# Performance work log

Hardware: AMD Instinct MI355X
Metric: run time of the kernel (lower is better)

Reference implementation:

```python
import jax, jax.numpy as jnp
import numpy as np

B, H, W, C = 64, 56, 56, 128
WIN, SHIFT, NH = 7, 3, 4
HD = C // NH
N = WIN * WIN
HID = 4 * C
EPS = 1e-5


def _rel_index():
    coords = np.stack(np.meshgrid(np.arange(WIN), np.arange(WIN), indexing='ij')).reshape(2, -1)
    rel = coords[:, :, None] - coords[:, None, :]
    rel = rel.transpose(1, 2, 0).astype(np.int64)
    rel[..., 0] += WIN - 1
    rel[..., 1] += WIN - 1
    rel[..., 0] *= 2 * WIN - 1
    return rel.sum(-1)  # [N, N]


def _attn_mask():
    img = np.zeros((H, W), dtype=np.float32)
    cnt = 0
    bounds = [(0, H - WIN), (H - WIN, H - SHIFT), (H - SHIFT, H)]
    for h0, h1 in bounds:
        for w0, w1 in bounds:
            img[h0:h1, w0:w1] = cnt
            cnt += 1
    mw = img.reshape(H // WIN, WIN, W // WIN, WIN).transpose(0, 2, 1, 3).reshape(-1, N)
    am = mw[:, None, :] - mw[:, :, None]
    return np.where(am != 0, -100.0, 0.0).astype(np.float32)  # [nW, N, N]


def setup_inputs() -> dict:
    key = jax.random.key(0)
    ks = jax.random.split(key, 16)
    s = lambda k, shp, f: (jax.random.normal(k, shp, jnp.float32) * f)
    return {
        'x': s(ks[0], (B, H * W, C), 1.0),
        'norm1_w': jnp.ones((C,), jnp.float32),
        'norm1_b': jnp.zeros((C,), jnp.float32),
        'qkv_w': s(ks[1], (3 * C, C), 0.02),
        'qkv_b': jnp.zeros((3 * C,), jnp.float32),
        'proj_w': s(ks[2], (C, C), 0.02),
        'proj_b': jnp.zeros((C,), jnp.float32),
        'norm2_w': jnp.ones((C,), jnp.float32),
        'norm2_b': jnp.zeros((C,), jnp.float32),
        'fc1_w': s(ks[3], (HID, C), 0.02),
        'fc1_b': jnp.zeros((HID,), jnp.float32),
        'fc2_w': s(ks[4], (C, HID), 0.02),
        'fc2_b': jnp.zeros((C,), jnp.float32),
        'bias_table': s(ks[5], ((2 * WIN - 1) ** 2, NH), 0.02),
        'attn_mask': jnp.asarray(_attn_mask()),
        'rel_index': jnp.asarray(_rel_index(), jnp.int32),
    }


def _ln(x, w, b):
    mu = x.mean(-1, keepdims=True)
    var = ((x - mu) ** 2).mean(-1, keepdims=True)
    return (x - mu) * jax.lax.rsqrt(var + EPS) * w + b


def reference(x, norm1_w, norm1_b, qkv_w, qkv_b, proj_w, proj_b,
              norm2_w, norm2_b, fc1_w, fc1_b, fc2_w, fc2_b,
              bias_table, attn_mask, rel_index):
    Bx, L, Cx = x.shape
    shortcut = x
    xn = _ln(x, norm1_w, norm1_b).reshape(Bx, H, W, Cx)
    xs = jnp.roll(xn, (-SHIFT, -SHIFT), axis=(1, 2))
    # window partition -> [B*nW, N, C]
    xw = xs.reshape(Bx, H // WIN, WIN, W // WIN, WIN, Cx).transpose(0, 1, 3, 2, 4, 5).reshape(-1, N, Cx)
    B_ = xw.shape[0]
    qkv = (xw @ qkv_w.T + qkv_b).reshape(B_, N, 3, NH, HD).transpose(2, 0, 3, 1, 4)
    q, k, v = qkv[0], qkv[1], qkv[2]
    q = q * (HD ** -0.5)
    attn = jnp.einsum('bhnd,bhmd->bhnm', q, k)  # [B_, NH, N, N]
    bias = bias_table[rel_index.reshape(-1)].reshape(N, N, NH).transpose(2, 0, 1)
    attn = attn + bias[None]
    nW = attn_mask.shape[0]
    attn = attn.reshape(B_ // nW, nW, NH, N, N) + attn_mask[None, :, None]
    attn = jax.nn.softmax(attn.reshape(B_, NH, N, N), axis=-1)
    out = jnp.einsum('bhnm,bhmd->bhnd', attn, v).transpose(0, 2, 1, 3).reshape(B_, N, Cx)
    out = out @ proj_w.T + proj_b
    # window reverse + roll back
    out = out.reshape(Bx, H // WIN, W // WIN, WIN, WIN, Cx).transpose(0, 1, 3, 2, 4, 5).reshape(Bx, H, W, Cx)
    out = jnp.roll(out, (SHIFT, SHIFT), axis=(1, 2)).reshape(Bx, L, Cx)
    x = shortcut + out
    h = _ln(x, norm2_w, norm2_b)
    h = jax.nn.gelu(h @ fc1_w.T + fc1_b, approximate=False) @ fc2_w.T + fc2_b
    return x + h
```

## Files before the change

kernel.cpp:

```cpp
#include <hip/hip_runtime.h>
#include <hip/hip_bf16.h>
#include <stdint.h>

typedef unsigned int uint;
typedef unsigned short ushort;
typedef short s16x8 __attribute__((ext_vector_type(8)));
typedef float f32x4 __attribute__((ext_vector_type(4)));

#define DEV static __device__ __forceinline__

DEV float bflo(uint u){ union{uint i;float f;} v; v.i = u<<16; return v.f; }
DEV float bfhi(uint u){ union{uint i;float f;} v; v.i = u & 0xffff0000u; return v.f; }
DEV float bf2f(ushort u){ union{uint i;float f;} v; v.i = ((uint)u)<<16; return v.f; }
DEV ushort f2bf(float f){ union{float f;uint i;} v; v.f=f; uint r=(v.i + 0x7fffu + ((v.i>>16)&1u))>>16; return (ushort)r; }

DEV f32x4 MFMA_BF(s16x8 a, s16x8 b, f32x4 c){
  return __builtin_amdgcn_mfma_f32_16x16x32_bf16(a, b, c, 0, 0, 0);
}

DEV float ld1(const void* b, int i, bool f32){
  return f32 ? ((const float*)b)[i] : bf2f(((const ushort*)b)[i]);
}
DEV ushort ld_bf(const void* b, int i, bool f32){
  return f32 ? f2bf(((const float*)b)[i]) : ((const ushort*)b)[i];
}
DEV void ld2(const void* b, int i, bool f32, float& a0, float& a1){
  if(f32){ float2 t = *(const float2*)((const float*)b + i); a0=t.x; a1=t.y; }
  else   { uint p = *(const uint*)((const ushort*)b + i); a0=bflo(p); a1=bfhi(p); }
}
DEV void ld8(const void* b, int i, bool f32, float* f){
  if(f32){
    const float* p = (const float*)b + i;
    float4 a0 = *(const float4*)p, a1 = *(const float4*)(p+4);
    f[0]=a0.x; f[1]=a0.y; f[2]=a0.z; f[3]=a0.w;
    f[4]=a1.x; f[5]=a1.y; f[6]=a1.z; f[7]=a1.w;
  } else {
    uint4 p = *(const uint4*)((const ushort*)b + i);
    f[0]=bflo(p.x); f[1]=bfhi(p.x); f[2]=bflo(p.y); f[3]=bfhi(p.y);
    f[4]=bflo(p.z); f[5]=bfhi(p.z); f[6]=bflo(p.w); f[7]=bfhi(p.w);
  }
}
DEV void st1(void* b, int i, bool f32, float v){
  if(f32) ((float*)b)[i] = v; else ((ushort*)b)[i] = f2bf(v);
}
DEV bool probe_f32(const void* normw){ return *(const uint*)normw == 0x3F800000u; }
DEV float clamp1k(float v){ return fminf(fmaxf(v, -1024.f), 1024.f); }

DEV float gelu_fast(float a){
  float t = a*(0.79788456080286536f + 0.035677408136300125f*a*a);
  float e = __expf(2.f*t);
  float th = 1.f - 2.f/(e+1.f);
  return 0.5f*a*(1.f+th);
}


__global__ void swin_prep(const void* __restrict__ n1w,
                          const void* __restrict__ qkvw, const void* __restrict__ projw,
                          const void* __restrict__ btab, const int* __restrict__ ridx,
                          const void* __restrict__ amask,
                          const void* __restrict__ fc1w, const void* __restrict__ fc2w,
                          ushort* __restrict__ qkvw_r, ushort* __restrict__ projw_r,
                          ushort* __restrict__ comb_t, ushort* __restrict__ amask_t,
                          ushort* __restrict__ fc1w_r, ushort* __restrict__ fc2w_r)
{
  const bool f32 = probe_f32(n1w);
  int idx=blockIdx.x*256+threadIdx.x;
  if(idx<49152){
    int j=idx&7, l=(idx>>3)&63, rest=idx>>9, ks=rest&3, nt=rest>>2;
    qkvw_r[idx]=ld_bf(qkvw, (nt*16+(l&15))*128 + ks*32 + (l>>4)*8 + j, f32);
  }
  if(idx<16384){
    int j=idx&7, l=(idx>>3)&63, rest=idx>>9, ks=rest&3, nt=rest>>2;
    projw_r[idx]=ld_bf(projw, (nt*16+(l&15))*128 + ks*32 + (l>>4)*8 + j, f32);
  }
  if(idx<65536){
    int j=idx&7, l=(idx>>3)&63, rest=idx>>9, ks=rest&3, nt=rest>>2;
    fc1w_r[idx]=ld_bf(fc1w, (nt*16+(l&15))*128 + ks*32 + (l>>4)*8 + j, f32);
  }
  if(idx<65536){
    int j=idx&7, l=(idx>>3)&63, rest=idx>>9, ks=rest&15, nt=rest>>4;
    fc2w_r[idx]=ld_bf(fc2w, (nt*16+(l&15))*512 + ks*32 + (l>>4)*8 + j, f32);
  }
  if(idx<12544){
    int hh=idx/3136, rm=idx-hh*3136, m=rm>>6, n=rm&63;
    comb_t[idx]=(n<49)?ld_bf(btab, ridx[n*49+m]*4+hh, f32):(ushort)0;
  }
  if(idx<200704){
    int w2=idx/3136, rm=idx-w2*3136, m=rm>>6, n=rm&63;
    amask_t[idx]=(n<49)?ld_bf(amask, (w2*49+n)*49+m, f32):(ushort)0;
  }
}

__global__ __launch_bounds__(512,4)
void swin_attn_mfma(const void* __restrict__ x,
                    const void* __restrict__ n1w, const void* __restrict__ n1b,
                    const void* __restrict__ qkvb, const void* __restrict__ projb,
                    const ushort* __restrict__ qkvw_r, const ushort* __restrict__ projw_r,
                    const ushort* __restrict__ comb_t, const ushort* __restrict__ amask_t,
                    void* __restrict__ y)
{
  __shared__ __align__(16) ushort smA[9216];
  __shared__ __align__(16) ushort smB[16896];
  const bool f32 = probe_f32(n1w);
  const int tid=threadIdx.x, lane=tid&63, wv=tid>>6;
  const int g=lane>>4, lr=lane&15;
  const int hi=wv&1, nh=wv>>1;
  const int widx=blockIdx.x, b=widx>>6, wi=widx&63, wh=wi>>3, ww=wi&7;
  const bool boundary=(wh==7)||(ww==7);

  {
    float w0,w1,c0,c1;
    ld2(n1w, 2*lane, f32, w0, w1);
    ld2(n1b, 2*lane, f32, c0, c1);
    float a0[7], a1[7];
    #pragma unroll
    for(int k=0;k<7;++k){
      int r=wv+8*k;
      if(r<49){
        int i=r/7, j=r-7*i;
        int hs=wh*7+i+3; if(hs>=56)hs-=56;
        int vs=ww*7+j+3; if(vs>=56)vs-=56;
        ld2(x, (b*3136+hs*56+vs)*128 + 2*lane, f32, a0[k], a1[k]);
      }
    }
    #pragma unroll
    for(int k=0;k<7;++k){
      int r=wv+8*k;
      if(r<49){
        float s=a0[k]+a1[k], q=a0[k]*a0[k]+a1[k]*a1[k];
        #pragma unroll
        for(int off=32;off;off>>=1){ s+=__shfl_xor(s,off); q+=__shfl_xor(q,off); }
        float mu=s*(1.f/128.f);
        float var=q*(1.f/128.f)-mu*mu;
        float rs=rsqrtf(var+1e-5f);
        smA[r*136+2*lane  ]=f2bf((a0[k]-mu)*rs*w0+c0);
        smA[r*136+2*lane+1]=f2bf((a1[k]-mu)*rs*w1+c1);
      }
    }
    for(int k=tid;k<15*136;k+=512) smA[49*136+k]=0;
  }
  __syncthreads();

  s16x8 af[2][4];
  #pragma unroll
  for(int i=0;i<2;++i)
    #pragma unroll
    for(int ks=0;ks<4;++ks)
      af[i][ks]=*(const s16x8*)&smA[((hi*2+i)*16+lr)*136 + ks*32 + g*8];
  __syncthreads();

  #pragma unroll 1
  for(int t=0;t<6;++t){
    int nt=nh*6+t;
    int col=nt*16+lr;
    s16x8 bf[4];
    #pragma unroll
    for(int ks=0;ks<4;++ks) bf[ks]=*(const s16x8*)&qkvw_r[(size_t)((nt*4+ks)*64+lane)*8];
    float bias=ld1(qkvb, col, f32);
    #pragma unroll
    for(int i=0;i<2;++i){
      int mt=hi*2+i;
      f32x4 acc={0.f,0.f,0.f,0.f};
      #pragma unroll
      for(int ks=0;ks<4;++ks) acc=MFMA_BF(af[i][ks],bf[ks],acc);
      if(nt<8){
        #pragma unroll
        for(int r=0;r<4;++r)
          smB[(mt*16+g*4+r)*264+col]=f2bf((acc[r]+bias)*0.17677669529663689f);
      } else if(nt<16){
        #pragma unroll
        for(int r=0;r<4;++r)
          smB[(mt*16+g*4+r)*264+col]=f2bf(acc[r]+bias);
      } else {
        int vd=col-256;
        ushort u[4];
        #pragma unroll
        for(int r=0;r<4;++r){
          int m=mt*16+g*4+r;
          u[r]=(m<49)?f2bf(acc[r]+bias):(ushort)0;
        }
        uint2 pk; pk.x=(uint)u[0]|((uint)u[1]<<16); pk.y=(uint)u[2]|((uint)u[3]<<16);
        *(uint2*)&smA[vd*72+mt*16+g*4]=pk;
      }
    }
  }
  __syncthreads();

  const int h=nh;
  f32x4 S[2][4];
  {
    s16x8 qa[2];
    #pragma unroll
    for(int i=0;i<2;++i) qa[i]=*(const s16x8*)&smB[((hi*2+i)*16+lr)*264 + h*32 + g*8];
    #pragma unroll
    for(int nt=0;nt<4;++nt){
      s16x8 kb=*(const s16x8*)&smB[(nt*16+lr)*264 + 128 + h*32 + g*8];
      #pragma unroll
      for(int i=0;i<2;++i){
        f32x4 z={0.f,0.f,0.f,0.f};
        S[i][nt]=MFMA_BF(qa[i],kb,z);
      }
    }
  }
  #pragma unroll
  for(int nt=0;nt<4;++nt){
    int m=nt*16+lr;
    if(m<49){
      #pragma unroll
      for(int i=0;i<2;++i){
        int n0=(hi*2+i)*16+g*4;
        uint2 cb=*(const uint2*)&comb_t[(size_t)(h*49+m)*64+n0];
        S[i][nt][0]+=bflo(cb.x); S[i][nt][1]+=bfhi(cb.x);
        S[i][nt][2]+=bflo(cb.y); S[i][nt][3]+=bfhi(cb.y);
      }
      if(boundary){
        #pragma unroll
        for(int i=0;i<2;++i){
          int n0=(hi*2+i)*16+g*4;
          uint2 mk=*(const uint2*)&amask_t[(size_t)(wi*49+m)*64+n0];
          S[i][nt][0]+=bflo(mk.x); S[i][nt][1]+=bfhi(mk.x);
          S[i][nt][2]+=bflo(mk.y); S[i][nt][3]+=bfhi(mk.y);
        }
      }
    } else {
      #pragma unroll
      for(int i=0;i<2;++i){
        #pragma unroll
        for(int r=0;r<4;++r) S[i][nt][r]=-3.0e4f;
      }
    }
  }
  float inv_[2][4];
  #pragma unroll
  for(int i=0;i<2;++i){
    #pragma unroll
    for(int r=0;r<4;++r){
      float v=fmaxf(fmaxf(S[i][0][r],S[i][1][r]),fmaxf(S[i][2][r],S[i][3][r]));
      v=fmaxf(v,__shfl_xor(v,1)); v=fmaxf(v,__shfl_xor(v,2));
      v=fmaxf(v,__shfl_xor(v,4)); v=fmaxf(v,__shfl_xor(v,8));
      #pragma unroll
      for(int nt=0;nt<4;++nt) S[i][nt][r]=__expf(S[i][nt][r]-v);
      float s=S[i][0][r]+S[i][1][r]+S[i][2][r]+S[i][3][r];
      s+=__shfl_xor(s,1); s+=__shfl_xor(s,2); s+=__shfl_xor(s,4); s+=__shfl_xor(s,8);
      inv_[i][r]=1.f/s;
    }
  }
  __syncthreads();

  #pragma unroll
  for(int nt=0;nt<4;++nt){
    int m=nt*16+lr;
    #pragma unroll
    for(int i=0;i<2;++i){
      #pragma unroll
      for(int r=0;r<4;++r)
        smB[((hi*2+i)*16+g*4+r)*264 + h*66 + m]=f2bf(S[i][nt][r]);
    }
  }
  __syncthreads();

  f32x4 O[2][2];
  {
    s16x8 vb[2][2];
    #pragma unroll
    for(int dt=0;dt<2;++dt)
      #pragma unroll
      for(int ks=0;ks<2;++ks)
        vb[dt][ks]=*(const s16x8*)&smA[(h*32+dt*16+lr)*72 + ks*32 + g*8];
    #pragma unroll
    for(int i=0;i<2;++i){
      s16x8 pa0=*(const s16x8*)&smB[((hi*2+i)*16+lr)*264 + h*66 + g*8];
      s16x8 pa1=*(const s16x8*)&smB[((hi*2+i)*16+lr)*264 + h*66 + 32 + g*8];
      #pragma unroll
      for(int dt=0;dt<2;++dt){
        f32x4 z={0.f,0.f,0.f,0.f};
        z=MFMA_BF(pa0,vb[dt][0],z);
        O[i][dt]=MFMA_BF(pa1,vb[dt][1],z);
      }
    }
  }
  __syncthreads();

  #pragma unroll
  for(int i=0;i<2;++i){
    #pragma unroll
    for(int dt=0;dt<2;++dt){
      int d=h*32+dt*16+lr;
      #pragma unroll
      for(int r=0;r<4;++r)
        smA[((hi*2+i)*16+g*4+r)*136 + d]=f2bf(O[i][dt][r]*inv_[i][r]);
    }
  }
  __syncthreads();

  {
    s16x8 oa[2][4];
    #pragma unroll
    for(int i=0;i<2;++i)
      #pragma unroll
      for(int ks=0;ks<4;++ks)
        oa[i][ks]=*(const s16x8*)&smA[((hi*2+i)*16+lr)*136 + ks*32 + g*8];
    #pragma unroll 1
    for(int t=0;t<2;++t){
      int nt=nh*2+t;
      int c=nt*16+lr;
      int   ga[2][4];
      float xres[2][4];
      #pragma unroll
      for(int i=0;i<2;++i){
        #pragma unroll
        for(int r=0;r<4;++r){
          int n=(hi*2+i)*16+g*4+r;
          if(n<49){
            int ii=n/7, jj=n-7*ii;
            int hh=wh*7+ii+3; if(hh>=56)hh-=56;
            int vv=ww*7+jj+3; if(vv>=56)vv-=56;
            ga[i][r]=(b*3136+hh*56+vv)*128+c;
            xres[i][r]=ld1(x, ga[i][r], f32);
          } else { ga[i][r]=-1; xres[i][r]=0.f; }
        }
      }
      s16x8 bfp[4];
      #pragma unroll
      for(int ks=0;ks<4;++ks) bfp[ks]=*(const s16x8*)&projw_r[(size_t)((nt*4+ks)*64+lane)*8];
      float pbv=ld1(projb, c, f32);
      #pragma unroll
      for(int i=0;i<2;++i){
        f32x4 acc={0.f,0.f,0.f,0.f};
        #pragma unroll
        for(int ks=0;ks<4;++ks) acc=MFMA_BF(oa[i][ks],bfp[ks],acc);
        #pragma unroll
        for(int r=0;r<4;++r){
          if(ga[i][r]>=0)
            st1(y, ga[i][r], f32, clamp1k(acc[r]+pbv+xres[i][r]));
        }
      }
    }
  }
}

__global__ __launch_bounds__(256,4)
void swin_mlp_mfma(void* __restrict__ y,
                   const void* __restrict__ n2w, const void* __restrict__ n2b,
                   const void* __restrict__ fc1b, const void* __restrict__ fc2b,
                   const ushort* __restrict__ fc1w_r, const ushort* __restrict__ fc2w_r)
{
  __shared__ __align__(16) ushort smH[64*264];
  const bool f32 = probe_f32(n2w);
  const int tid=threadIdx.x, lane=tid&63, wv=tid>>6;
  const int g=lane>>4, lr=lane&15;
  const int row0=blockIdx.x*64;

  {
    float w0,w1,c0,c1;
    ld2(n2w, 2*lane, f32, w0, w1);
    ld2(n2b, 2*lane, f32, c0, c1);
    for(int r=wv;r<64;r+=4){
      float a0,a1; ld2(y, (row0+r)*128 + 2*lane, f32, a0, a1);
      float s=a0+a1, q=a0*a0+a1*a1;
      #pragma unroll
      for(int off=32;off;off>>=1){ s+=__shfl_xor(s,off); q+=__shfl_xor(q,off); }
      float mu=s*(1.f/128.f);
      float var=q*(1.f/128.f)-mu*mu;
      float rs=rsqrtf(var+1e-5f);
      smH[r*136+2*lane  ]=f2bf((a0-mu)*rs*w0+c0);
      smH[r*136+2*lane+1]=f2bf((a1-mu)*rs*w1+c1);
    }
  }
  __syncthreads();

  s16x8 af[4][4];
  #pragma unroll
  for(int mt=0;mt<4;++mt)
    #pragma unroll
    for(int ks=0;ks<4;++ks)
      af[mt][ks]=*(const s16x8*)&smH[(mt*16+lr)*136 + ks*32 + g*8];
  __syncthreads();

  f32x4 acc2[4][2];
  #pragma unroll
  for(int mt=0;mt<4;++mt)
    #pragma unroll
    for(int tn=0;tn<2;++tn) acc2[mt][tn]=(f32x4){0.f,0.f,0.f,0.f};

  #pragma unroll 1
  for(int half=0;half<2;++half){
    #pragma unroll 1
    for(int t=0;t<4;++t){
      int nt=half*16 + wv*4 + t;
      int col=nt*16+lr;
      s16x8 bf[4];
      #pragma unroll
      for(int ks=0;ks<4;++ks) bf[ks]=*(const s16x8*)&fc1w_r[(size_t)((nt*4+ks)*64+lane)*8];
      float bias=ld1(fc1b, col, f32);
      int lcol=col-half*256;
      #pragma unroll
      for(int mt=0;mt<4;++mt){
        f32x4 acc={0.f,0.f,0.f,0.f};
        #pragma unroll
        for(int ks=0;ks<4;++ks) acc=MFMA_BF(af[mt][ks],bf[ks],acc);
        #pragma unroll
        for(int r=0;r<4;++r)
          smH[(mt*16+g*4+r)*264 + lcol]=f2bf(gelu_fast(acc[r]+bias));
      }
    }
    __syncthreads();
    #pragma unroll 1
    for(int ksl=0;ksl<8;++ksl){
      s16x8 am[4];
      #pragma unroll
      for(int mt=0;mt<4;++mt) am[mt]=*(const s16x8*)&smH[(mt*16+lr)*264 + ksl*32 + g*8];
      s16x8 bn[2];
      #pragma unroll
      for(int tn=0;tn<2;++tn)
        bn[tn]=*(const s16x8*)&fc2w_r[(size_t)(((wv*2+tn)*16 + half*8+ksl)*64+lane)*8];
      #pragma unroll
      for(int mt=0;mt<4;++mt)
        #pragma unroll
        for(int tn=0;tn<2;++tn) acc2[mt][tn]=MFMA_BF(am[mt],bn[tn],acc2[mt][tn]);
    }
    __syncthreads();
  }

  #pragma unroll
  for(int tn=0;tn<2;++tn){
    int col=(wv*2+tn)*16+lr;
    float fb=ld1(fc2b, col, f32);
    #pragma unroll
    for(int mt=0;mt<4;++mt){
      #pragma unroll
      for(int r=0;r<4;++r){
        int gr=row0 + mt*16+g*4+r;
        float v=acc2[mt][tn][r]+fb+ld1(y, gr*128+col, f32);
        st1(y, gr*128+col, f32, v);
      }
    }
  }
}

__global__ __launch_bounds__(256,2)
void swin_mlp(void* __restrict__ y,
              const void* __restrict__ n2w, const void* __restrict__ n2b,
              const void* __restrict__ fc1w, const void* __restrict__ fc1b,
              const void* __restrict__ fc2w, const void* __restrict__ fc2b)
{
  __shared__ float sY[16*128];
  __shared__ float sH[16*512];
  const bool f32 = probe_f32(n2w);
  const int tid=threadIdx.x, lane=tid&63, wave=tid>>6;
  const int g0=blockIdx.x*16;
  {
    float w0,w1,c0,c1;
    ld2(n2w, 2*lane, f32, w0, w1);
    ld2(n2b, 2*lane, f32, c0, c1);
    for(int r=wave;r<16;r+=4){
      float a0,a1; ld2(y, (g0+r)*128+2*lane, f32, a0, a1);
      float s=a0+a1, q=a0*a0+a1*a1;
      #pragma unroll
      for(int off=32;off;off>>=1){ s+=__shfl_xor(s,off); q+=__shfl_xor(q,off); }
      float mu=s*(1.f/128.f), var=q*(1.f/128.f)-mu*mu, rs=rsqrtf(var+1e-5f);
      sY[r*128+2*lane  ]=(a0-mu)*rs*w0+c0;
      sY[r*128+2*lane+1]=(a1-mu)*rs*w1+c1;
    }
  }
  __syncthreads();
  #pragma unroll 1
  for(int pass=0;pass<2;++pass){
    int col=tid+256*pass;
    float acc[16];
    #pragma unroll
    for(int r=0;r<16;++r) acc[r]=0.f;
    for(int k8=0;k8<16;++k8){
      float wf[8]; ld8(fc1w, col*128+k8*8, f32, wf);
      const float* abase=&sY[k8*8];
      #pragma unroll
      for(int r=0;r<16;++r){
        const float* ar=abase+r*128;
        float4 a0=*(const float4*)ar, a1=*(const float4*)(ar+4);
        acc[r]+=a0.x*wf[0]+a0.y*wf[1]+a0.z*wf[2]+a0.w*wf[3]
              +a1.x*wf[4]+a1.y*wf[5]+a1.z*wf[6]+a1.w*wf[7];
      }
    }
    float fb=ld1(fc1b, col, f32);
    #pragma unroll
    for(int r=0;r<16;++r){
      float a=acc[r]+fb;
      sH[r*512+col]=0.5f*a*(1.f+erff(a*0.70710678118654752f));
    }
  }
  __syncthreads();
  {
    const int col=tid&127, rg=tid>>7;
    float acc[8];
    #pragma unroll
    for(int r=0;r<8;++r) acc[r]=0.f;
    for(int k8=0;k8<64;++k8){
      float wf[8]; ld8(fc2w, col*512+k8*8, f32, wf);
      const float* abase=&sH[rg*8*512+k8*8];
      #pragma unroll
      for(int r=0;r<8;++r){
        const float* ar=abase+r*512;
        float4 a0=*(const float4*)ar, a1=*(const float4*)(ar+4);
        acc[r]+=a0.x*wf[0]+a0.y*wf[1]+a0.z*wf[2]+a0.w*wf[3]
              +a1.x*wf[4]+a1.y*wf[5]+a1.z*wf[6]+a1.w*wf[7];
      }
    }
    float fb=ld1(fc2b, col, f32);
    #pragma unroll
    for(int r=0;r<8;++r){
      int gr=g0+rg*8+r;
      float v=acc[r]+fb+ld1(y, gr*128+col, f32);
      st1(y, gr*128+col, f32, v);
    }
  }
}

constexpr int LDA = 132;
constexpr int LDQ = 392;

__global__ __launch_bounds__(256,2)
void swin_attn(const void* __restrict__ x,
               const void* __restrict__ n1w, const void* __restrict__ n1b,
               const void* __restrict__ qkvw, const void* __restrict__ qkvb,
               const void* __restrict__ projw, const void* __restrict__ projb,
               const void* __restrict__ btab, const void* __restrict__ amask,
               const int* __restrict__ ridx, void* __restrict__ y)
{
  __shared__ float  sA[49*LDA];
  __shared__ ushort sQ[49*LDQ];
  const bool f32 = probe_f32(n1w);
  const int tid=threadIdx.x, lane=tid&63, wave=tid>>6;
  const int widx=blockIdx.x, b=widx>>6, wi=widx&63, wh=wi>>3, ww=wi&7;
  {
    float w0,w1,c0,c1;
    ld2(n1w, 2*lane, f32, w0, w1);
    ld2(n1b, 2*lane, f32, c0, c1);
    for(int r=wave;r<49;r+=4){
      int i=r/7, j=r-7*(r/7);
      int hs=wh*7+i+3; if(hs>=56) hs-=56;
      int vs=ww*7+j+3; if(vs>=56) vs-=56;
      int base=(b*3136 + hs*56 + vs)*128;
      float a0,a1; ld2(x, base+2*lane, f32, a0, a1);
      float s=a0+a1, q=a0*a0+a1*a1;
      #pragma unroll
      for(int off=32;off;off>>=1){ s+=__shfl_xor(s,off); q+=__shfl_xor(q,off); }
      float mu=s*(1.f/128.f);
      float var=q*(1.f/128.f)-mu*mu;
      float rs=rsqrtf(var+1e-5f);
      sA[r*LDA+2*lane  ]=(a0-mu)*rs*w0+c0;
      sA[r*LDA+2*lane+1]=(a1-mu)*rs*w1+c1;
    }
  }
  __syncthreads();
  #pragma unroll 1
  for(int pass=0;pass<2;++pass){
    int col=tid+256*pass;
    if(col<384){
      float acc[49];
      #pragma unroll
      for(int r=0;r<49;++r) acc[r]=0.f;
      for(int k8=0;k8<16;++k8){
        float wf[8]; ld8(qkvw, col*128+k8*8, f32, wf);
        const float* abase=&sA[k8*8];
        #pragma unroll
        for(int r=0;r<49;++r){
          const float* ar=abase+r*LDA;
          float4 a0=*(const float4*)ar;
          float4 a1=*(const float4*)(ar+4);
          acc[r]+=a0.x*wf[0]+a0.y*wf[1]+a0.z*wf[2]+a0.w*wf[3]
                +a1.x*wf[4]+a1.y*wf[5]+a1.z*wf[6]+a1.w*wf[7];
        }
      }
      float bias=ld1(qkvb, col, f32);
      float scale=(col<128)?0.17677669529663689f:1.f;
      #pragma unroll
      for(int r=0;r<49;++r) sQ[r*LDQ+col]=f2bf((acc[r]+bias)*scale);
    }
  }
  __syncthreads();
  if(lane<49){
    const int head=wave, n=lane;
    float qv[32];
    {
      const ushort* qr=&sQ[n*LDQ+head*32];
      #pragma unroll
      for(int c=0;c<4;++c){
        uint4 p=*(const uint4*)(qr+c*8);
        qv[c*8+0]=bflo(p.x); qv[c*8+1]=bfhi(p.x);
        qv[c*8+2]=bflo(p.y); qv[c*8+3]=bfhi(p.y);
        qv[c*8+4]=bflo(p.z); qv[c*8+5]=bfhi(p.z);
        qv[c*8+6]=bflo(p.w); qv[c*8+7]=bfhi(p.w);
      }
    }
    float sc[49];
    #pragma unroll
    for(int m=0;m<49;++m){
      const ushort* kr=&sQ[m*LDQ+128+head*32];
      float acc=0.f;
      #pragma unroll
      for(int c=0;c<4;++c){
        uint4 p=*(const uint4*)(kr+c*8);
        acc+=qv[c*8+0]*bflo(p.x)+qv[c*8+1]*bfhi(p.x)
            +qv[c*8+2]*bflo(p.y)+qv[c*8+3]*bfhi(p.y)
            +qv[c*8+4]*bflo(p.z)+qv[c*8+5]*bfhi(p.z)
            +qv[c*8+6]*bflo(p.w)+qv[c*8+7]*bfhi(p.w);
      }
      int rr=ridx[n*49+m];
      acc+=ld1(btab, rr*4+head, f32);
      acc+=ld1(amask, (wi*49+n)*49+m, f32);
      sc[m]=acc;
    }
    float mx=sc[0];
    #pragma unroll
    for(int m=1;m<49;++m) mx=fmaxf(mx,sc[m]);
    float sum=0.f;
    #pragma unroll
    for(int m=0;m<49;++m){ sc[m]=__expf(sc[m]-mx); sum+=sc[m]; }
    float inv=1.f/sum;
    float ov[32];
    #pragma unroll
    for(int d=0;d<32;++d) ov[d]=0.f;
    #pragma unroll
    for(int m=0;m<49;++m){
      const ushort* vr=&sQ[m*LDQ+256+head*32];
      float pm=sc[m];
      #pragma unroll
      for(int c=0;c<4;++c){
        uint4 p=*(const uint4*)(vr+c*8);
        ov[c*8+0]+=pm*bflo(p.x); ov[c*8+1]+=pm*bfhi(p.x);
        ov[c*8+2]+=pm*bflo(p.y); ov[c*8+3]+=pm*bfhi(p.y);
        ov[c*8+4]+=pm*bflo(p.z); ov[c*8+5]+=pm*bfhi(p.z);
        ov[c*8+6]+=pm*bflo(p.w); ov[c*8+7]+=pm*bfhi(p.w);
      }
    }
    #pragma unroll
    for(int d=0;d<32;++d) sA[n*LDA+head*32+d]=ov[d]*inv;
  }
  __syncthreads();
  {
    const int col=tid&127, rh=tid>>7;
    const int r0=rh*25, nr=rh?24:25;
    float acc[25];
    #pragma unroll
    for(int r=0;r<25;++r) acc[r]=0.f;
    for(int k8=0;k8<16;++k8){
      float wf[8]; ld8(projw, col*128+k8*8, f32, wf);
      const float* abase=&sA[r0*LDA+k8*8];
      #pragma unroll
      for(int r=0;r<25;++r){
        if(r<nr){
          const float* ar=abase+r*LDA;
          float4 a0=*(const float4*)ar;
          float4 a1=*(const float4*)(ar+4);
          acc[r]+=a0.x*wf[0]+a0.y*wf[1]+a0.z*wf[2]+a0.w*wf[3]
                +a1.x*wf[4]+a1.y*wf[5]+a1.z*wf[6]+a1.w*wf[7];
        }
      }
    }
    float pb=ld1(projb, col, f32);
    #pragma unroll
    for(int r=0;r<25;++r){
      if(r<nr){
        int row=r0+r;
        int i=row/7, j=row-7*(row/7);
        int hh=wh*7+i+3; if(hh>=56) hh-=56;
        int vv=ww*7+j+3; if(vv>=56) vv-=56;
        int gidx=(b*3136+hh*56+vv)*128+col;
        st1(y, gidx, f32, acc[r]+pb+ld1(x, gidx, f32));
      }
    }
  }
}

extern "C" void kernel_launch(void* const* d_in, const int* in_sizes, int n_in,
                              void* d_out, int out_size, void* d_ws, size_t ws_size,
                              hipStream_t stream)
{
  const void* x    =d_in[0];
  const void* n1w  =d_in[1];
  const void* n1b  =d_in[2];
  const void* qkvw =d_in[3];
  const void* qkvb =d_in[4];
  const void* projw=d_in[5];
  const void* projb=d_in[6];
  const void* n2w  =d_in[7];
  const void* n2b  =d_in[8];
  const void* fc1w =d_in[9];
  const void* fc1b =d_in[10];
  const void* fc2w =d_in[11];
  const void* fc2b =d_in[12];
  const void* btab =d_in[13];
  const void* amask=d_in[14];
  const int*  ridx =(const int*)d_in[15];

  const size_t NEED = 819712;
  if(ws_size >= NEED){
    char* w = (char*)d_ws;
    ushort* qkvw_r = (ushort*)(w + 0);
    ushort* projw_r= (ushort*)(w + 98304);
    ushort* comb_t = (ushort*)(w + 131072);
    ushort* amask_t= (ushort*)(w + 156160);
    ushort* fc1w_r = (ushort*)(w + 557568);
    ushort* fc2w_r = (ushort*)(w + 688640);
    swin_prep<<<784,256,0,stream>>>(n1w,qkvw,projw,btab,ridx,amask,fc1w,fc2w,
                                    qkvw_r,projw_r,comb_t,amask_t,fc1w_r,fc2w_r);
    swin_attn_mfma<<<4096,512,0,stream>>>(x,n1w,n1b,qkvb,projb,
                                          qkvw_r,projw_r,comb_t,amask_t,d_out);
    swin_mlp_mfma<<<3136,256,0,stream>>>(d_out,n2w,n2b,fc1b,fc2b,fc1w_r,fc2w_r);
  } else {
    swin_attn<<<4096,256,0,stream>>>(x,n1w,n1b,qkvw,qkvb,projw,projb,btab,amask,ridx,d_out);
    swin_mlp<<<12544,256,0,stream>>>(d_out,n2w,n2b,fc1w,fc1b,fc2w,fc2b);
  }
}
```

Baseline: 343.8 us.

## Use packed bf16 conversion, batch LN loads, raise occupancy hint, drop a barrier

Replaces the software float-to-bf16 rounding with the hardware v_cvt_pk_bf16_f32 instruction and writes packed pairs to shared memory. The MLP kernel's LayerNorm now issues all 16 row loads before reducing them, to overlap global memory latency. It also partially unrolls the QKV, fc1 and fc2 loops and raises the attention kernel's launch-bounds occupancy hint from 4 to 6. A barrier between writing and reading the softmax probabilities is removed, since each wave only reads back the rows and columns it wrote itself. The higher occupancy hint pressures register allocation and could cause spills, and shared-memory use likely still caps blocks per CU.

Result: slower. 377.9 us (+9.9%).

```diff
diff --git a/kernel.cpp b/kernel.cpp
--- a/kernel.cpp
+++ b/kernel.cpp
@@ -12,7 +12,12 @@
 DEV float bflo(uint u){ union{uint i;float f;} v; v.i = u<<16; return v.f; }
 DEV float bfhi(uint u){ union{uint i;float f;} v; v.i = u & 0xffff0000u; return v.f; }
 DEV float bf2f(ushort u){ union{uint i;float f;} v; v.i = ((uint)u)<<16; return v.f; }
-DEV ushort f2bf(float f){ union{float f;uint i;} v; v.f=f; uint r=(v.i + 0x7fffu + ((v.i>>16)&1u))>>16; return (ushort)r; }
+DEV uint f2bf2(float lo, float hi){
+  uint r;
+  asm("v_cvt_pk_bf16_f32 %0, %1, %2" : "=v"(r) : "v"(lo), "v"(hi));
+  return r;
+}
+DEV ushort f2bf(float f){ return (ushort)f2bf2(f,f); }
 
 DEV f32x4 MFMA_BF(s16x8 a, s16x8 b, f32x4 c){
   return __builtin_amdgcn_mfma_f32_16x16x32_bf16(a, b, c, 0, 0, 0);
@@ -91,7 +96,7 @@
   }
 }
 
-__global__ __launch_bounds__(512,4)
+__global__ __launch_bounds__(512,6)
 void swin_attn_mfma(const void* __restrict__ x,
                     const void* __restrict__ n1w, const void* __restrict__ n1b,
                     const void* __restrict__ qkvb, const void* __restrict__ projb,
@@ -133,8 +138,7 @@
         float mu=s*(1.f/128.f);
         float var=q*(1.f/128.f)-mu*mu;
         float rs=rsqrtf(var+1e-5f);
-        smA[r*136+2*lane  ]=f2bf((a0[k]-mu)*rs*w0+c0);
-        smA[r*136+2*lane+1]=f2bf((a1[k]-mu)*rs*w1+c1);
+        *(uint*)&smA[r*136+2*lane]=f2bf2((a0[k]-mu)*rs*w0+c0,(a1[k]-mu)*rs*w1+c1);
       }
     }
     for(int k=tid;k<15*136;k+=512) smA[49*136+k]=0;
@@ -149,7 +153,7 @@
       af[i][ks]=*(const s16x8*)&smA[((hi*2+i)*16+lr)*136 + ks*32 + g*8];
   __syncthreads();
 
-  #pragma unroll 1
+  #pragma unroll 2
   for(int t=0;t<6;++t){
     int nt=nh*6+t;
     int col=nt*16+lr;
@@ -173,13 +177,11 @@
           smB[(mt*16+g*4+r)*264+col]=f2bf(acc[r]+bias);
       } else {
         int vd=col-256;
-        ushort u[4];
-        #pragma unroll
-        for(int r=0;r<4;++r){
-          int m=mt*16+g*4+r;
-          u[r]=(m<49)?f2bf(acc[r]+bias):(ushort)0;
-        }
-        uint2 pk; pk.x=(uint)u[0]|((uint)u[1]<<16); pk.y=(uint)u[2]|((uint)u[3]<<16);
+        float v0=(mt*16+g*4+0<49)?(acc[0]+bias):0.f;
+        float v1=(mt*16+g*4+1<49)?(acc[1]+bias):0.f;
+        float v2=(mt*16+g*4+2<49)?(acc[2]+bias):0.f;
+        float v3=(mt*16+g*4+3<49)?(acc[3]+bias):0.f;
+        uint2 pk; pk.x=f2bf2(v0,v1); pk.y=f2bf2(v2,v3);
         *(uint2*)&smA[vd*72+mt*16+g*4]=pk;
       }
     }
@@ -257,7 +259,6 @@
         smB[((hi*2+i)*16+g*4+r)*264 + h*66 + m]=f2bf(S[i][nt][r]);
     }
   }
-  __syncthreads();
 
   f32x4 O[2][2];
   {
@@ -355,16 +356,22 @@
     float w0,w1,c0,c1;
     ld2(n2w, 2*lane, f32, w0, w1);
     ld2(n2b, 2*lane, f32, c0, c1);
-    for(int r=wv;r<64;r+=4){
-      float a0,a1; ld2(y, (row0+r)*128 + 2*lane, f32, a0, a1);
-      float s=a0+a1, q=a0*a0+a1*a1;
+    float a0[16], a1[16];
+    #pragma unroll
+    for(int k=0;k<16;++k){
+      int r=wv+4*k;
+      ld2(y, (row0+r)*128 + 2*lane, f32, a0[k], a1[k]);
+    }
+    #pragma unroll
+    for(int k=0;k<16;++k){
+      int r=wv+4*k;
+      float s=a0[k]+a1[k], q=a0[k]*a0[k]+a1[k]*a1[k];
       #pragma unroll
       for(int off=32;off;off>>=1){ s+=__shfl_xor(s,off); q+=__shfl_xor(q,off); }
       float mu=s*(1.f/128.f);
       float var=q*(1.f/128.f)-mu*mu;
       float rs=rsqrtf(var+1e-5f);
-      smH[r*136+2*lane  ]=f2bf((a0-mu)*rs*w0+c0);
-      smH[r*136+2*lane+1]=f2bf((a1-mu)*rs*w1+c1);
+      *(uint*)&smH[r*136+2*lane]=f2bf2((a0[k]-mu)*rs*w0+c0,(a1[k]-mu)*rs*w1+c1);
     }
   }
   __syncthreads();
@@ -385,7 +392,7 @@
 
   #pragma unroll 1
   for(int half=0;half<2;++half){
-    #pragma unroll 1
+    #pragma unroll 2
     for(int t=0;t<4;++t){
       int nt=half*16 + wv*4 + t;
       int col=nt*16+lr;
@@ -405,7 +412,7 @@
       }
     }
     __syncthreads();
-    #pragma unroll 1
+    #pragma unroll 2
     for(int ksl=0;ksl<8;++ksl){
       s16x8 am[4];
       #pragma unroll
```
